# Performance work log

Hardware: AMD Instinct MI355X
Metric: run time of the kernel (lower is better)

Reference implementation:

```python
import jax, jax.numpy as jnp
import numpy as np

N = 50000      # num_labels (nodes)
HID = 64       # hidden_dim
HEADS = 4
CH = 16        # hidden_dim // 4 per head
R = 4          # relations
E = 200000     # edges per relation
DEPTH = 2
SLOPE = 0.2    # GATv2 leaky_relu negative slope
EPS = 1e-5     # LayerNorm eps


def layer_norm(x, g, b):
    mu = jnp.mean(x, axis=-1, keepdims=True)
    var = jnp.mean((x - mu) ** 2, axis=-1, keepdims=True)
    return (x - mu) / jnp.sqrt(var + EPS) * g + b


def setup_inputs() -> dict:
    key = jax.random.key(0)
    ks = jax.random.split(key, 8)
    # edges with src != dst (PyG remove_self_loops is then a no-op)
    src = jax.random.randint(ks[0], (R, E), 0, N, dtype=jnp.int32)
    off = jax.random.randint(ks[1], (R, E), 1, N, dtype=jnp.int32)
    dst = ((src + off) % N).astype(jnp.int32)
    edge_index = jnp.stack([src, dst], axis=1)  # [R, 2, E]
    s = 1.0 / np.sqrt(HID)
    return {
        "label_embeddings": jax.random.normal(ks[2], (N, HID), jnp.float32) * 0.5,
        "entry_w": jax.random.normal(ks[3], (HID, HID), jnp.float32) * s,
        "entry_b": jnp.zeros((HID,), jnp.float32),
        "entry_ln_g": jnp.ones((HID,), jnp.float32),
        "entry_ln_b": jnp.zeros((HID,), jnp.float32),
        "conv_wl": jax.random.normal(ks[4], (DEPTH, R, HID, HEADS * CH), jnp.float32) * s,
        "conv_wr": jax.random.normal(ks[5], (DEPTH, R, HID, HEADS * CH), jnp.float32) * s,
        "conv_att": jax.random.normal(ks[6], (DEPTH, R, HEADS, CH), jnp.float32) * (1.0 / np.sqrt(CH)),
        "conv_bias": jnp.zeros((DEPTH, R, HEADS * CH), jnp.float32),
        "norm_g": jnp.ones((HID,), jnp.float32),
        "norm_b": jnp.zeros((HID,), jnp.float32),
        "edge_index": edge_index,
    }


def _gatv2_layer(x, wl, wr, att, bias, src, dst):
    """One GATv2Conv over one relation. x:[N,HID]; returns [N, HEADS*CH]."""
    xl = (x @ wl).reshape(N, HEADS, CH)  # source transform
    xr = (x @ wr).reshape(N, HEADS, CH)  # target transform
    m = xl[src] + xr[dst]                          # [E+N, HEADS, CH]
    e = jnp.einsum('ehc,hc->eh', jax.nn.leaky_relu(m, SLOPE), att)  # [E+N, HEADS]
    # segment softmax over incoming edges of each dst node
    emax = jax.ops.segment_max(e, dst, num_segments=N)  # [N, HEADS]
    a = jnp.exp(e - emax[dst])
    denom = jax.ops.segment_sum(a, dst, num_segments=N)
    alpha = a / denom[dst]                          # every node has a self-loop -> denom > 0
    msg = xl[src] * alpha[..., None]                # [E+N, HEADS, CH]
    out = jax.ops.segment_sum(msg, dst, num_segments=N).reshape(N, HEADS * CH)
    return out + bias


def reference(label_embeddings, entry_w, entry_b, entry_ln_g, entry_ln_b,
              conv_wl, conv_wr, conv_att, conv_bias, norm_g, norm_b, edge_index):
    x = jax.nn.gelu(layer_norm(label_embeddings @ entry_w + entry_b, entry_ln_g, entry_ln_b),
                    approximate=False)
    loop = jnp.arange(N, dtype=edge_index.dtype)
    for layer in range(DEPTH):
        outs = []
        for r in range(R):
            src = jnp.concatenate([edge_index[r, 0], loop])  # add self-loops (PyG default)
            dst = jnp.concatenate([edge_index[r, 1], loop])
            outs.append(_gatv2_layer(x, conv_wl[layer, r], conv_wr[layer, r],
                                     conv_att[layer, r], conv_bias[layer, r], src, dst))
        x = sum(outs) / R                              # HeteroConv aggr='mean'
        x = layer_norm(jax.nn.gelu(x, approximate=False), norm_g, norm_b)  # dropout = identity (eval)
    return x
```

## Files before the change

kernel.cpp:

```cpp
#include <hip/hip_runtime.h>
#include <hip/hip_bf16.h>

#define NN 50000
#define RR 4
#define EE 200000

typedef __hip_bfloat16 bf16;
typedef __attribute__((ext_vector_type(8))) short short8;
typedef __attribute__((ext_vector_type(4))) float float4v;
typedef __attribute__((ext_vector_type(2))) float float2v;

__device__ __forceinline__ unsigned short f2bu(float v) {
    bf16 h = __float2bfloat16(v);
    return *(unsigned short*)&h;
}
__device__ __forceinline__ float ldf(const void* p, int i, int isbf) {
    return isbf ? __bfloat162float(((const bf16*)p)[i]) : ((const float*)p)[i];
}
__device__ __forceinline__ int dtype_isbf(const void* lg) {
    return ((const unsigned*)lg)[0] == 0x3F803F80u;
}
__device__ __forceinline__ float gelu_exact(float x) {
    return 0.5f * x * (1.0f + erff(x * 0.70710678118654752f));
}
__device__ __forceinline__ float2v bp2(unsigned u) {
    float2v f;
    f.x = __uint_as_float(u << 16);
    f.y = __uint_as_float(u & 0xffff0000u);
    return f;
}
__device__ __forceinline__ float2v lrelu2(float2v m) {
    float2v s = m * 0.2f;
    float2v r;
    r.x = fmaxf(m.x, s.x);
    r.y = fmaxf(m.y, s.y);
    return r;
}

#define PW_ENTRY_W 0
#define PW_ENTRY_B 4096
#define PW_LN_G    4160
#define PW_LN_B    4224
#define PW_WL      4288
#define PW_ATT     69824
#define PW_BIAS    70336
#define PW_NG      70848
#define PW_NB      70912
#define PW_TOT     70976

#define WT_ELEMS (2 * RR * 128 * 64)
#define SCAN_N (RR * NN)
#define NSB 196

#define HIST_BLOCKS 32
#define RANGE_N 6250
#define CVT_BLOCKS 18
#define ENTRY_BLOCKS 625
#define ENTRY_WAVES 10000
__global__ __launch_bounds__(1024) void mega_k(const int* __restrict__ ei,
                                               int* __restrict__ cnt,
                                               unsigned char* __restrict__ slot8,
                                               const void* __restrict__ emb,
                                               const void* ew, const void* eb,
                                               const void* lg, const void* lb,
                                               const void* wl, const void* wr,
                                               const void* at, const void* bi,
                                               const void* ng, const void* nb,
                                               float* __restrict__ P,
                                               bf16* __restrict__ WT,
                                               bf16* __restrict__ xout) {
    int b = blockIdx.x;
    int t = threadIdx.x;
    int isbf = dtype_isbf(lg);
    if (b < HIST_BLOCKS) {
        __shared__ unsigned hc[RANGE_N];
        int r = b >> 3, rg = b & 7;
        for (int i = t; i < RANGE_N; i += 1024) hc[i] = 0u;
        __syncthreads();
        const uint4* dst4 = (const uint4*)(ei + r * 2 * EE + EE);
        unsigned base = rg * RANGE_N;
        unsigned char* sl = slot8 + (size_t)r * EE;
        for (int q = t; q < EE / 4; q += 1024) {
            uint4 d4 = dst4[q];
            int e = q * 4;
            unsigned x;
            x = d4.x - base; if (x < RANGE_N) sl[e + 0] = (unsigned char)atomicAdd(&hc[x], 1u);
            x = d4.y - base; if (x < RANGE_N) sl[e + 1] = (unsigned char)atomicAdd(&hc[x], 1u);
            x = d4.z - base; if (x < RANGE_N) sl[e + 2] = (unsigned char)atomicAdd(&hc[x], 1u);
            x = d4.w - base; if (x < RANGE_N) sl[e + 3] = (unsigned char)atomicAdd(&hc[x], 1u);
        }
        __syncthreads();
        int* cp = cnt + r * NN + base;
        for (int i = t; i < RANGE_N; i += 1024) cp[i] = (int)hc[i];
        return;
    }
    if (b < HIST_BLOCKS + CVT_BLOCKS) {
#pragma unroll
        for (int j = 0; j < 4; j++) {
            int i = (b - HIST_BLOCKS) * 4096 + j * 1024 + t;
            if (i < WT_ELEMS) {
                int k = i & 63;
                int c = (i >> 6) & 127;
                int lr = i >> 13;
                float v = (c < 64) ? ldf(wl, (lr * 64 + k) * 64 + c, isbf)
                                   : ldf(wr, (lr * 64 + k) * 64 + (c - 64), isbf);
                WT[i] = __float2bfloat16(v);
            }
            if (i < PW_TOT) {
                const void* src = nullptr;
                int off = 0;
                if (i < PW_ENTRY_B)      { src = ew; off = i - PW_ENTRY_W; }
                else if (i < PW_LN_G)    { src = eb; off = i - PW_ENTRY_B; }
                else if (i < PW_LN_B)    { src = lg; off = i - PW_LN_G; }
                else if (i < PW_WL)      { src = lb; off = i - PW_LN_B; }
                else if (i < PW_ATT)     { src = nullptr; }
                else if (i < PW_BIAS)    { src = at; off = i - PW_ATT; }
                else if (i < PW_NG)      { src = bi; off = i - PW_BIAS; }
                else if (i < PW_NB)      { src = ng; off = i - PW_NG; }
                else                     { src = nb; off = i - PW_NB; }
                if (src) P[i] = ldf(src, off, isbf);
            }
        }
        return;
    }
    int wv = (b - HIST_BLOCKS - CVT_BLOCKS) * 16 + (t >> 6);
    int c = t & 63;
    for (int j = 0; j < 5; j++) {
        int node = wv + j * ENTRY_WAVES;
        float ev = ldf(emb, node * 64 + c, isbf);
        float acc = 0.f;
#pragma unroll 8
        for (int k = 0; k < 64; k++) {
            float xv = __shfl(ev, k, 64);
            acc += xv * ldf(ew, k * 64 + c, isbf);
        }
        acc += ldf(eb, c, isbf);
        float s = acc;
#pragma unroll
        for (int m = 1; m < 64; m <<= 1) s += __shfl_xor(s, m, 64);
        float mu = s * (1.f / 64.f);
        float d = acc - mu;
        float vs = d * d;
#pragma unroll
        for (int m = 1; m < 64; m <<= 1) vs += __shfl_xor(vs, m, 64);
        float var = vs * (1.f / 64.f);
        float y = d * rsqrtf(var + 1e-5f) * ldf(lg, c, isbf) + ldf(lb, c, isbf);
        xout[node * 64 + c] = __float2bfloat16(gelu_exact(y));
    }
}

__global__ __launch_bounds__(256) void scanA_k(const int* __restrict__ cnt,
                                               int* __restrict__ bsum) {
    int b = blockIdx.x, t = threadIdx.x;
    int s = 0;
#pragma unroll
    for (int j = 0; j < 4; j++) {
        int i = b * 1024 + j * 256 + t;
        if (i < SCAN_N) s += cnt[i];
    }
#pragma unroll
    for (int m = 1; m < 64; m <<= 1) s += __shfl_xor(s, m, 64);
    __shared__ int ws[4];
    if ((t & 63) == 0) ws[t >> 6] = s;
    __syncthreads();
    if (t == 0) bsum[b] = ws[0] + ws[1] + ws[2] + ws[3];
}

__global__ void scanB_k(int* __restrict__ bsum, int* __restrict__ rp) {
    int l = threadIdx.x;
    int i0 = l * 4;
    int v0 = (i0 + 0 < NSB) ? bsum[i0 + 0] : 0;
    int v1 = (i0 + 1 < NSB) ? bsum[i0 + 1] : 0;
    int v2 = (i0 + 2 < NSB) ? bsum[i0 + 2] : 0;
    int v3 = (i0 + 3 < NSB) ? bsum[i0 + 3] : 0;
    int ts = v0 + v1 + v2 + v3;
    int inc = ts;
#pragma unroll
    for (int m = 1; m < 64; m <<= 1) {
        int y = __shfl_up(inc, m, 64);
        if (l >= m) inc += y;
    }
    int run = inc - ts;
    if (i0 + 0 < NSB) { bsum[i0 + 0] = run; run += v0; }
    if (i0 + 1 < NSB) { bsum[i0 + 1] = run; run += v1; }
    if (i0 + 2 < NSB) { bsum[i0 + 2] = run; run += v2; }
    if (i0 + 3 < NSB) { bsum[i0 + 3] = run; run += v3; }
    if (l == 63) rp[SCAN_N] = inc;
}

__global__ __launch_bounds__(256) void scanC_k(const int* __restrict__ cnt,
                                               const int* __restrict__ bsum,
                                               int* __restrict__ rp) {
    int b = blockIdx.x, t = threadIdx.x;
    int i0 = b * 1024 + t * 4;
    int v0 = (i0 + 0 < SCAN_N) ? cnt[i0 + 0] : 0;
    int v1 = (i0 + 1 < SCAN_N) ? cnt[i0 + 1] : 0;
    int v2 = (i0 + 2 < SCAN_N) ? cnt[i0 + 2] : 0;
    int v3 = (i0 + 3 < SCAN_N) ? cnt[i0 + 3] : 0;
    int ts = v0 + v1 + v2 + v3;
    int lane = t & 63, w = t >> 6;
    int inc = ts;
#pragma unroll
    for (int m = 1; m < 64; m <<= 1) {
        int y = __shfl_up(inc, m, 64);
        if (lane >= m) inc += y;
    }
    __shared__ int ws[4];
    if (lane == 63) ws[w] = inc;
    __syncthreads();
    int run = bsum[b];
    for (int k = 0; k < w; k++) run += ws[k];
    run += inc - ts;
    if (i0 + 0 < SCAN_N) { rp[i0 + 0] = run; run += v0; }
    if (i0 + 1 < SCAN_N) { rp[i0 + 1] = run; run += v1; }
    if (i0 + 2 < SCAN_N) { rp[i0 + 2] = run; run += v2; }
    if (i0 + 3 < SCAN_N) { rp[i0 + 3] = run; run += v3; }
}

#define GR 80
__global__ __launch_bounds__(256) void gemm_m(const bf16* __restrict__ X,
                                              const bf16* __restrict__ WTlayer,
                                              bf16* __restrict__ xlB,
                                              bf16* __restrict__ xrB,
                                              const int* __restrict__ ei,
                                              const unsigned char* __restrict__ slot8,
                                              const int* __restrict__ rp,
                                              unsigned short* __restrict__ col,
                                              int scatBlk) {
    int bx = blockIdx.x;
    int r = blockIdx.y;
    if (bx < scatBlk) {
        const int* eis = ei + r * 2 * EE;
#pragma unroll
        for (int j = 0; j < 4; j++) {
            int e = bx * 1024 + j * 256 + threadIdx.x;
            if (e < EE) {
                int s = eis[e];
                int d = eis[EE + e];
                int p = slot8[(size_t)r * EE + e];
                col[rp[r * NN + d] + p] = (unsigned short)s;
            }
        }
        return;
    }
    const short* Xs = (const short*)X;
    const short* WT = (const short*)(WTlayer + (size_t)r * 8192);
    bf16* xl = xlB + (size_t)r * NN * 64;
    bf16* xr = xrB + (size_t)r * NN * 64;

    __shared__ float sh[16 * 132];
    int t = threadIdx.x;
    int w = t >> 6;
    int lane = t & 63;
    int m = lane & 15, kq = lane >> 4;
    int row0 = (bx - scatBlk) * GR;

    short8 b0[2], b1[2];
    int c0t[2];
#pragma unroll
    for (int tile = 0; tile < 2; tile++) {
        int ct = w * 2 + tile;
        int c0 = ct * 16 + m;
        c0t[tile] = c0;
        const short* bp = WT + c0 * 64 + kq * 8;
        b0[tile] = *(const short8*)bp;
        b1[tile] = *(const short8*)(bp + 32);
    }

    const short* ap = Xs + (row0 + m) * 64 + kq * 8;
    short8 a0 = *(const short8*)ap;
    short8 a1 = *(const short8*)(ap + 32);

    for (int g = 0; g < 5; g++) {
        short8 na0, na1;
        if (g < 4) {
            const short* np = ap + (g + 1) * 16 * 64;
            na0 = *(const short8*)np;
            na1 = *(const short8*)(np + 32);
        }
#pragma unroll
        for (int tile = 0; tile < 2; tile++) {
            float4v acc = {0.f, 0.f, 0.f, 0.f};
            asm volatile(
                "v_mfma_f32_16x16x32_bf16 %0, %1, %2, %0\n\t"
                "v_mfma_f32_16x16x32_bf16 %0, %3, %4, %0\n\t"
                "s_nop 7\n\t"
                "s_nop 7"
                : "+v"(acc)
                : "v"(a0), "v"(b0[tile]), "v"(a1), "v"(b1[tile]));
#pragma unroll
            for (int i = 0; i < 4; i++) sh[(kq * 4 + i) * 132 + c0t[tile]] = acc[i];
        }
        __syncthreads();
        {
            int row = t >> 4, cg = (t & 15) * 8;
            float v0 = sh[row * 132 + cg + 0], v1 = sh[row * 132 + cg + 1];
            float v2 = sh[row * 132 + cg + 2], v3 = sh[row * 132 + cg + 3];
            float v4 = sh[row * 132 + cg + 4], v5 = sh[row * 132 + cg + 5];
            float v6 = sh[row * 132 + cg + 6], v7 = sh[row * 132 + cg + 7];
            uint4 u;
            u.x = ((unsigned)f2bu(v1) << 16) | f2bu(v0);
            u.y = ((unsigned)f2bu(v3) << 16) | f2bu(v2);
            u.z = ((unsigned)f2bu(v5) << 16) | f2bu(v4);
            u.w = ((unsigned)f2bu(v7) << 16) | f2bu(v6);
            size_t grow = row0 + g * 16 + row;
            if (cg < 64) *(uint4*)&xl[grow * 64 + cg] = u;
            else         *(uint4*)&xr[grow * 64 + (cg - 64)] = u;
        }
        __syncthreads();
        a0 = na0; a1 = na1;
    }
}

__device__ __forceinline__ void edge_accum(uint4 u0, uint4 u1, bool act,
                                           const float2v at2[8], const float2v xr2[8],
                                           float2v A2[8], float& D) {
    float2v x2[8];
    x2[0] = bp2(u0.x); x2[1] = bp2(u0.y); x2[2] = bp2(u0.z); x2[3] = bp2(u0.w);
    x2[4] = bp2(u1.x); x2[5] = bp2(u1.y); x2[6] = bp2(u1.z); x2[7] = bp2(u1.w);
    float2v t2 = (float2v){0.f, 0.f};
#pragma unroll
    for (int i = 0; i < 8; i++)
        t2 = t2 + lrelu2(x2[i] + xr2[i]) * at2[i];
    float tt = t2.x + t2.y;
    float p = act ? exp2f(tt) : 0.f;
    D += p;
    float2v p2 = (float2v){p, p};
#pragma unroll
    for (int i = 0; i < 8; i++) A2[i] = A2[i] + p2 * x2[i];
}

__global__ __launch_bounds__(256) void aggfin_k(const bf16* __restrict__ xlB,
                                                const bf16* __restrict__ xrB,
                                                const float* __restrict__ attL,
                                                const float* __restrict__ biasL,
                                                const int* __restrict__ rp,
                                                const unsigned short* __restrict__ col,
                                                const float* __restrict__ P,
                                                const void* __restrict__ lg,
                                                void* __restrict__ outp,
                                                int finalOut) {
    __shared__ float shRes[RR][4][68];
    int t = threadIdx.x;
    int r = t >> 6;
    int lane = t & 63;
    int nodeBase = blockIdx.x * 4;
    int nn = lane >> 4, es = (lane >> 2) & 3, h = lane & 3;
    int node = nodeBase + nn;

    const unsigned* xl = (const unsigned*)(xlB + (size_t)r * NN * 64);
    const unsigned* xr = (const unsigned*)(xrB + (size_t)r * NN * 64);
    const float* att = attL + r * 64;
    const float* bias = biasL + r * 64;

    int idx = r * NN + node;
    int base = rp[idx];
    int cn = rp[idx + 1] - base;
    const uint4* qr = (const uint4*)(xr + (size_t)node * 32 + h * 8);
    uint4 r0 = qr[0], r1 = qr[1];

    const unsigned short* bucket = col + base;
    int c0raw = (es > 0) ? (int)bucket[es - 1] : node;
    int c1raw = (int)bucket[es + 3];

    unsigned s0 = (unsigned)c0raw < (unsigned)NN ? (unsigned)c0raw : (unsigned)(NN - 1);
    unsigned s1 = (unsigned)c1raw < (unsigned)NN ? (unsigned)c1raw : (unsigned)(NN - 1);
    const uint4* q0 = (const uint4*)(xl + (size_t)s0 * 32 + h * 8);
    uint4 u0 = q0[0], u1 = q0[1];
    const uint4* q1 = (const uint4*)(xl + (size_t)s1 * 32 + h * 8);
    uint4 w0 = q1[0], w1 = q1[1];

    float2v at2[8], xr2[8];
    {
        const float4* apv = (const float4*)(att + h * 16);
#pragma unroll
        for (int i = 0; i < 4; i++) {
            float4 a = apv[i];
            at2[2 * i].x = a.x * 1.44269504f; at2[2 * i].y = a.y * 1.44269504f;
            at2[2 * i + 1].x = a.z * 1.44269504f; at2[2 * i + 1].y = a.w * 1.44269504f;
        }
        xr2[0] = bp2(r0.x); xr2[1] = bp2(r0.y); xr2[2] = bp2(r0.z); xr2[3] = bp2(r0.w);
        xr2[4] = bp2(r1.x); xr2[5] = bp2(r1.y); xr2[6] = bp2(r1.z); xr2[7] = bp2(r1.w);
    }
    int total = cn + 1;
    int kmax = total;
    kmax = max(kmax, __shfl_xor(kmax, 16, 64));
    kmax = max(kmax, __shfl_xor(kmax, 32, 64));

    float2v A2[8];
#pragma unroll
    for (int i = 0; i < 8; i++) A2[i] = (float2v){0.f, 0.f};
    float D = 0.f;

    edge_accum(u0, u1, es < total, at2, xr2, A2, D);
    edge_accum(w0, w1, es + 4 < total, at2, xr2, A2, D);

    for (int k = es + 8; k < kmax; k += 4) {
        bool act = k < total;
        int sr = act ? (int)bucket[k - 1] : node;
        const uint4* q = (const uint4*)(xl + (size_t)sr * 32 + h * 8);
        uint4 t0 = q[0], t1 = q[1];
        edge_accum(t0, t1, act, at2, xr2, A2, D);
    }

    D += __shfl_xor(D, 4, 64);
    D += __shfl_xor(D, 8, 64);
#pragma unroll
    for (int i = 0; i < 8; i++) {
        A2[i].x += __shfl_xor(A2[i].x, 4, 64);
        A2[i].x += __shfl_xor(A2[i].x, 8, 64);
        A2[i].y += __shfl_xor(A2[i].y, 4, 64);
        A2[i].y += __shfl_xor(A2[i].y, 8, 64);
    }
    if (es == 0) {
        float inv = __builtin_amdgcn_rcpf(D);
        const float4* bp = (const float4*)(bias + h * 16);
        float* dst = &shRes[r][nn][h * 16];
#pragma unroll
        for (int i = 0; i < 4; i++) {
            float4 b = bp[i];
            dst[4 * i + 0] = A2[2 * i].x * inv + b.x;
            dst[4 * i + 1] = A2[2 * i].y * inv + b.y;
            dst[4 * i + 2] = A2[2 * i + 1].x * inv + b.z;
            dst[4 * i + 3] = A2[2 * i + 1].y * inv + b.w;
        }
    }
    __syncthreads();
    int wn = t >> 6, c = t & 63;
    float v = shRes[0][wn][c] + shRes[1][wn][c] + shRes[2][wn][c] + shRes[3][wn][c];
    v = gelu_exact(v * 0.25f);
    float s = v;
#pragma unroll
    for (int m = 1; m < 64; m <<= 1) s += __shfl_xor(s, m, 64);
    float mu = s * (1.f / 64.f);
    float d = v - mu;
    float vs = d * d;
#pragma unroll
    for (int m = 1; m < 64; m <<= 1) vs += __shfl_xor(vs, m, 64);
    float var = vs * (1.f / 64.f);
    float y = d * rsqrtf(var + 1e-5f) * P[PW_NG + c] + P[PW_NB + c];
    size_t o = (size_t)(nodeBase + wn) * 64 + c;
    if (!finalOut) {
        ((bf16*)outp)[o] = __float2bfloat16(y);
    } else {
        if (dtype_isbf(lg)) ((bf16*)outp)[o] = __float2bfloat16(y);
        else                ((float*)outp)[o] = y;
    }
}

extern "C" void kernel_launch(void* const* d_in, const int* in_sizes, int n_in,
                              void* d_out, int out_size, void* d_ws, size_t ws_size,
                              hipStream_t stream) {
    const void* emb = d_in[0];
    const void* lg  = d_in[3];
    const int*  ei  = (const int*)d_in[11];

    const size_t BUF = (size_t)NN * 64;

    bf16* X   = (bf16*)d_ws;
    bf16* XL  = X + BUF;
    bf16* XR  = XL + RR * BUF;
    bf16* WT  = XR + RR * BUF;
    float* P  = (float*)(WT + WT_ELEMS);
    int* cnt  = (int*)(P + PW_TOT);
    int* rp   = cnt + SCAN_N;
    int* bsum = rp + SCAN_N + 1;
    unsigned short* col = (unsigned short*)(bsum + 256);
    unsigned char* slot8 = (unsigned char*)(col + RR * EE + 64);

    mega_k<<<HIST_BLOCKS + CVT_BLOCKS + ENTRY_BLOCKS, 1024, 0, stream>>>(
        ei, cnt, slot8, emb, d_in[1], d_in[2], d_in[3], d_in[4], d_in[5], d_in[6],
        d_in[7], d_in[8], d_in[9], d_in[10], P, WT, X);

    scanA_k<<<NSB, 256, 0, stream>>>(cnt, bsum);
    scanB_k<<<1, 64, 0, stream>>>(bsum, rp);
    scanC_k<<<NSB, 256, 0, stream>>>(cnt, bsum, rp);

    int nodeBlocks = NN / 4;

    gemm_m<<<dim3(196 + 625, RR), 256, 0, stream>>>(
        X, WT, XL, XR, ei, slot8, rp, col, 196);
    aggfin_k<<<nodeBlocks, 256, 0, stream>>>(
        XL, XR, P + PW_ATT, P + PW_BIAS, rp, col, P, lg, (void*)X, 0);

    gemm_m<<<dim3(625, RR), 256, 0, stream>>>(
        X, WT + (size_t)RR * 8192, XL, XR, ei, slot8, rp, col, 0);
    aggfin_k<<<nodeBlocks, 256, 0, stream>>>(
        XL, XR, P + PW_ATT + RR * 64, P + PW_BIAS + RR * 64, rp, col, P, lg, d_out, 1);
}
```

Baseline: 306.7 us.

## Drop slot8 buffer; fold range sums into histogram and use single-pass scan

The histogram blocks now produce per-range totals, so the three-kernel scan collapses into one 32-block scan kernel. The per-edge slot byte array goes away. CSR fill instead reruns a shared-memory atomic counting pass per destination range (16 blocks per relation), each block reading all edges of its relation. This removes two launches and the slot8 writes and reads, at the cost of every scatter block reading the full edge list. Col order within a segment is nondeterministic, but it was already atomic-ordered before.

After: 531.1 us. 1.73x slower.

```diff
diff --git a/kernel.cpp b/kernel.cpp
--- a/kernel.cpp
+++ b/kernel.cpp
@@ -50,16 +50,16 @@
 
 #define WT_ELEMS (2 * RR * 128 * 64)
 #define SCAN_N (RR * NN)
-#define NSB 196
+#define NRANGE 32
+#define RANGE_N 6250
 
 #define HIST_BLOCKS 32
-#define RANGE_N 6250
 #define CVT_BLOCKS 18
 #define ENTRY_BLOCKS 625
 #define ENTRY_WAVES 10000
 __global__ __launch_bounds__(1024) void mega_k(const int* __restrict__ ei,
                                                int* __restrict__ cnt,
-                                               unsigned char* __restrict__ slot8,
+                                               int* __restrict__ rangeSum,
                                                const void* __restrict__ emb,
                                                const void* ew, const void* eb,
                                                const void* lg, const void* lb,
@@ -74,24 +74,37 @@
     int isbf = dtype_isbf(lg);
     if (b < HIST_BLOCKS) {
         __shared__ unsigned hc[RANGE_N];
+        __shared__ unsigned wsum[16];
         int r = b >> 3, rg = b & 7;
         for (int i = t; i < RANGE_N; i += 1024) hc[i] = 0u;
         __syncthreads();
         const uint4* dst4 = (const uint4*)(ei + r * 2 * EE + EE);
         unsigned base = rg * RANGE_N;
-        unsigned char* sl = slot8 + (size_t)r * EE;
         for (int q = t; q < EE / 4; q += 1024) {
             uint4 d4 = dst4[q];
-            int e = q * 4;
             unsigned x;
-            x = d4.x - base; if (x < RANGE_N) sl[e + 0] = (unsigned char)atomicAdd(&hc[x], 1u);
-            x = d4.y - base; if (x < RANGE_N) sl[e + 1] = (unsigned char)atomicAdd(&hc[x], 1u);
-            x = d4.z - base; if (x < RANGE_N) sl[e + 2] = (unsigned char)atomicAdd(&hc[x], 1u);
-            x = d4.w - base; if (x < RANGE_N) sl[e + 3] = (unsigned char)atomicAdd(&hc[x], 1u);
+            x = d4.x - base; if (x < RANGE_N) atomicAdd(&hc[x], 1u);
+            x = d4.y - base; if (x < RANGE_N) atomicAdd(&hc[x], 1u);
+            x = d4.z - base; if (x < RANGE_N) atomicAdd(&hc[x], 1u);
+            x = d4.w - base; if (x < RANGE_N) atomicAdd(&hc[x], 1u);
         }
         __syncthreads();
         int* cp = cnt + r * NN + base;
-        for (int i = t; i < RANGE_N; i += 1024) cp[i] = (int)hc[i];
+        unsigned s = 0;
+        for (int i = t; i < RANGE_N; i += 1024) {
+            unsigned v = hc[i];
+            cp[i] = (int)v;
+            s += v;
+        }
+#pragma unroll
+        for (int m = 1; m < 64; m <<= 1) s += __shfl_xor(s, m, 64);
+        if ((t & 63) == 0) wsum[t >> 6] = s;
+        __syncthreads();
+        if (t == 0) {
+            unsigned tot = 0;
+            for (int k = 0; k < 16; k++) tot += wsum[k];
+            rangeSum[b] = (int)tot;
+        }
         return;
     }
     if (b < HIST_BLOCKS + CVT_BLOCKS) {
@@ -149,107 +162,88 @@
     }
 }
 
-__global__ __launch_bounds__(256) void scanA_k(const int* __restrict__ cnt,
-                                               int* __restrict__ bsum) {
-    int b = blockIdx.x, t = threadIdx.x;
-    int s = 0;
-#pragma unroll
-    for (int j = 0; j < 4; j++) {
-        int i = b * 1024 + j * 256 + t;
-        if (i < SCAN_N) s += cnt[i];
-    }
-#pragma unroll
-    for (int m = 1; m < 64; m <<= 1) s += __shfl_xor(s, m, 64);
-    __shared__ int ws[4];
-    if ((t & 63) == 0) ws[t >> 6] = s;
+__global__ __launch_bounds__(256) void scan_k(const int* __restrict__ cnt,
+                                              const int* __restrict__ rangeSum,
+                                              int* __restrict__ rp) {
+    int b = blockIdx.x;
+    int t = threadIdx.x;
+    __shared__ int rs[NRANGE];
+    __shared__ int wpre[4];
+    if (t < NRANGE) rs[t] = rangeSum[t];
     __syncthreads();
-    if (t == 0) bsum[b] = ws[0] + ws[1] + ws[2] + ws[3];
-}
-
-__global__ void scanB_k(int* __restrict__ bsum, int* __restrict__ rp) {
-    int l = threadIdx.x;
-    int i0 = l * 4;
-    int v0 = (i0 + 0 < NSB) ? bsum[i0 + 0] : 0;
-    int v1 = (i0 + 1 < NSB) ? bsum[i0 + 1] : 0;
-    int v2 = (i0 + 2 < NSB) ? bsum[i0 + 2] : 0;
-    int v3 = (i0 + 3 < NSB) ? bsum[i0 + 3] : 0;
-    int ts = v0 + v1 + v2 + v3;
-    int inc = ts;
-#pragma unroll
-    for (int m = 1; m < 64; m <<= 1) {
-        int y = __shfl_up(inc, m, 64);
-        if (l >= m) inc += y;
-    }
-    int run = inc - ts;
-    if (i0 + 0 < NSB) { bsum[i0 + 0] = run; run += v0; }
-    if (i0 + 1 < NSB) { bsum[i0 + 1] = run; run += v1; }
-    if (i0 + 2 < NSB) { bsum[i0 + 2] = run; run += v2; }
-    if (i0 + 3 < NSB) { bsum[i0 + 3] = run; run += v3; }
-    if (l == 63) rp[SCAN_N] = inc;
-}
-
-__global__ __launch_bounds__(256) void scanC_k(const int* __restrict__ cnt,
-                                               const int* __restrict__ bsum,
-                                               int* __restrict__ rp) {
-    int b = blockIdx.x, t = threadIdx.x;
-    int i0 = b * 1024 + t * 4;
-    int v0 = (i0 + 0 < SCAN_N) ? cnt[i0 + 0] : 0;
-    int v1 = (i0 + 1 < SCAN_N) ? cnt[i0 + 1] : 0;
-    int v2 = (i0 + 2 < SCAN_N) ? cnt[i0 + 2] : 0;
-    int v3 = (i0 + 3 < SCAN_N) ? cnt[i0 + 3] : 0;
-    int ts = v0 + v1 + v2 + v3;
+    int base = 0;
+    for (int j = 0; j < b; j++) base += rs[j];
+    const int V = 25;
+    int i0 = t * V;
+    int gbase = b * RANGE_N;
+    int v[V];
+    int tsum = 0;
+#pragma unroll
+    for (int k = 0; k < V; k++) {
+        int i = i0 + k;
+        v[k] = (i < RANGE_N) ? cnt[gbase + i] : 0;
+        tsum += v[k];
+    }
     int lane = t & 63, w = t >> 6;
-    int inc = ts;
+    int inc = tsum;
 #pragma unroll
     for (int m = 1; m < 64; m <<= 1) {
         int y = __shfl_up(inc, m, 64);
         if (lane >= m) inc += y;
     }
-    __shared__ int ws[4];
-    if (lane == 63) ws[w] = inc;
+    if (lane == 63) wpre[w] = inc;
     __syncthreads();
-    int run = bsum[b];
-    for (int k = 0; k < w; k++) run += ws[k];
-    run += inc - ts;
-    if (i0 + 0 < SCAN_N) { rp[i0 + 0] = run; run += v0; }
-    if (i0 + 1 < SCAN_N) { rp[i0 + 1] = run; run += v1; }
-    if (i0 + 2 < SCAN_N) { rp[i0 + 2] = run; run += v2; }
-    if (i0 + 3 < SCAN_N) { rp[i0 + 3] = run; run += v3; }
+    int run = base;
+    for (int k = 0; k < w; k++) run += wpre[k];
+    run += inc - tsum;
+#pragma unroll
+    for (int k = 0; k < V; k++) {
+        int i = i0 + k;
+        if (i < RANGE_N) rp[gbase + i] = run;
+        run += v[k];
+    }
+    if (b == 0 && t == 0) rp[SCAN_N] = RR * EE;
 }
 
 #define GR 80
+#define RANGE2 3125
 __global__ __launch_bounds__(256) void gemm_m(const bf16* __restrict__ X,
                                               const bf16* __restrict__ WTlayer,
                                               bf16* __restrict__ xlB,
                                               bf16* __restrict__ xrB,
                                               const int* __restrict__ ei,
-                                              const unsigned char* __restrict__ slot8,
                                               const int* __restrict__ rp,
                                               unsigned short* __restrict__ col,
                                               int scatBlk) {
+    __shared__ unsigned smem[RANGE2 + 64];
     int bx = blockIdx.x;
     int r = blockIdx.y;
+    int t = threadIdx.x;
     if (bx < scatBlk) {
-        const int* eis = ei + r * 2 * EE;
-#pragma unroll
-        for (int j = 0; j < 4; j++) {
-            int e = bx * 1024 + j * 256 + threadIdx.x;
-            if (e < EE) {
-                int s = eis[e];
-                int d = eis[EE + e];
-                int p = slot8[(size_t)r * EE + e];
-                col[rp[r * NN + d] + p] = (unsigned short)s;
-            }
+        unsigned* hc = smem;
+        for (int i = t; i < RANGE2; i += 256) hc[i] = 0u;
+        __syncthreads();
+        const uint4* src4 = (const uint4*)(ei + r * 2 * EE);
+        const uint4* dst4 = (const uint4*)(ei + r * 2 * EE + EE);
+        unsigned base = bx * RANGE2;
+        const int* rpr = rp + r * NN;
+        for (int q = t; q < EE / 4; q += 256) {
+            uint4 d4 = dst4[q];
+            uint4 s4 = src4[q];
+            unsigned x;
+            x = d4.x - base; if (x < RANGE2) { unsigned p = atomicAdd(&hc[x], 1u); col[rpr[d4.x] + p] = (unsigned short)s4.x; }
+            x = d4.y - base; if (x < RANGE2) { unsigned p = atomicAdd(&hc[x], 1u); col[rpr[d4.y] + p] = (unsigned short)s4.y; }
+            x = d4.z - base; if (x < RANGE2) { unsigned p = atomicAdd(&hc[x], 1u); col[rpr[d4.z] + p] = (unsigned short)s4.z; }
+            x = d4.w - base; if (x < RANGE2) { unsigned p = atomicAdd(&hc[x], 1u); col[rpr[d4.w] + p] = (unsigned short)s4.w; }
         }
         return;
     }
+    float* sh = (float*)smem;
     const short* Xs = (const short*)X;
     const short* WT = (const short*)(WTlayer + (size_t)r * 8192);
     bf16* xl = xlB + (size_t)r * NN * 64;
     bf16* xr = xrB + (size_t)r * NN * 64;
 
-    __shared__ float sh[16 * 132];
-    int t = threadIdx.x;
     int w = t >> 6;
     int lane = t & 63;
     int m = lane & 15, kq = lane >> 4;
@@ -464,27 +458,24 @@
     float* P  = (float*)(WT + WT_ELEMS);
     int* cnt  = (int*)(P + PW_TOT);
     int* rp   = cnt + SCAN_N;
-    int* bsum = rp + SCAN_N + 1;
-    unsigned short* col = (unsigned short*)(bsum + 256);
-    unsigned char* slot8 = (unsigned char*)(col + RR * EE + 64);
+    int* rangeSum = rp + SCAN_N + 1;
+    unsigned short* col = (unsigned short*)(rangeSum + 64);
 
     mega_k<<<HIST_BLOCKS + CVT_BLOCKS + ENTRY_BLOCKS, 1024, 0, stream>>>(
-        ei, cnt, slot8, emb, d_in[1], d_in[2], d_in[3], d_in[4], d_in[5], d_in[6],
+        ei, cnt, rangeSum, emb, d_in[1], d_in[2], d_in[3], d_in[4], d_in[5], d_in[6],
         d_in[7], d_in[8], d_in[9], d_in[10], P, WT, X);
 
-    scanA_k<<<NSB, 256, 0, stream>>>(cnt, bsum);
-    scanB_k<<<1, 64, 0, stream>>>(bsum, rp);
-    scanC_k<<<NSB, 256, 0, stream>>>(cnt, bsum, rp);
+    scan_k<<<NRANGE, 256, 0, stream>>>(cnt, rangeSum, rp);
 
     int nodeBlocks = NN / 4;
 
-    gemm_m<<<dim3(196 + 625, RR), 256, 0, stream>>>(
-        X, WT, XL, XR, ei, slot8, rp, col, 196);
+    gemm_m<<<dim3(16 + 625, RR), 256, 0, stream>>>(
+        X, WT, XL, XR, ei, rp, col, 16);
     aggfin_k<<<nodeBlocks, 256, 0, stream>>>(
         XL, XR, P + PW_ATT, P + PW_BIAS, rp, col, P, lg, (void*)X, 0);
 
     gemm_m<<<dim3(625, RR), 256, 0, stream>>>(
-        X, WT + (size_t)RR * 8192, XL, XR, ei, slot8, rp, col, 0);
+        X, WT + (size_t)RR * 8192, XL, XR, ei, rp, col, 0);
     aggfin_k<<<nodeBlocks, 256, 0, stream>>>(
         XL, XR, P + PW_ATT + RR * 64, P + PW_BIAS + RR * 64, rp, col, P, lg, d_out, 1);
 }
```
